# Performance work log

Hardware: AMD Instinct MI355X
Metric: run time of the kernel (lower is better)

The kernel has to match this reference:

```python
import jax, jax.numpy as jnp
import numpy as np

B, N, D_IN, D_OUT = 4, 2048, 1024, 1024


def setup_inputs() -> dict:
    key = jax.random.key(0)
    k0, k1, k2, k3 = jax.random.split(key, 4)
    x = jax.random.normal(k0, (B, N, D_IN), dtype=jnp.float32)
    # torch Linear weight is [out, in]; store transposed [in, out] for x @ W
    W_query = jax.random.normal(k1, (D_IN, D_OUT), dtype=jnp.float32) * (D_IN ** -0.5)
    W_key = jax.random.normal(k2, (D_IN, D_OUT), dtype=jnp.float32) * (D_IN ** -0.5)
    W_value = jax.random.normal(k3, (D_IN, D_OUT), dtype=jnp.float32) * (D_IN ** -0.5)
    return {"x": x, "W_query": W_query, "W_key": W_key, "W_value": W_value}


def reference(x, W_query, W_key, W_value):
    # x: [B, N, D_IN]
    num_tokens = x.shape[1]
    embed_dim = x.shape[2]  # NB: original scales by INPUT embed dim
    q = jnp.einsum('bnd,de->bne', x, W_query)  # [B, N, D_OUT]
    k = jnp.einsum('bnd,de->bne', x, W_key)
    v = jnp.einsum('bnd,de->bne', x, W_value)
    scores = jnp.einsum('bqe,bke->bqk', q, k)  # [B, N, N]
    idx = jnp.arange(num_tokens)
    causal_mask = idx[None, :] > idx[:, None]  # True above diagonal
    scores = jnp.where(causal_mask[None, :, :], -jnp.inf, scores)
    scale = jnp.asarray(embed_dim, scores.dtype) ** 0.5
    attn = jax.nn.softmax(scores / scale, axis=-1)  # dropout p=0 (eval)
    context = jnp.einsum('bqk,bke->bqe', attn, v)  # [B, N, D_OUT]
    return context
```

## Files before the change

### kernel.cpp

```cpp
#include <hip/hip_runtime.h>


typedef __attribute__((ext_vector_type(8))) _Float16 half8;
typedef __attribute__((ext_vector_type(4))) _Float16 half4v;
typedef __attribute__((ext_vector_type(4))) float floatx4;

#define AS1 __attribute__((address_space(1)))
#define AS3 __attribute__((address_space(3)))

__device__ __forceinline__ void load16_lds(void* lds, const void* g) {
  __builtin_amdgcn_global_load_lds((AS1 void*)g, (AS3 void*)lds, 16, 0, 0);
}


__global__ __launch_bounds__(256)
void conv_f32_f16(const float* __restrict__ in, _Float16* __restrict__ out,
                  float* __restrict__ l) {
  if (blockIdx.x < 8192) {
    const int i = (blockIdx.x * 256 + threadIdx.x) << 2;
    float4 v = *(const float4*)(in + i);
    half4v o = { (_Float16)v.x, (_Float16)v.y, (_Float16)v.z, (_Float16)v.w };
    *(half4v*)(out + i) = o;
  } else {
    const int i = ((blockIdx.x - 8192) * 256 + threadIdx.x) << 2;
    *(float4*)(l + i) = float4{0.f, 0.f, 0.f, 0.f};
  }
}

__global__ __launch_bounds__(256)
void transpose_w(const float* __restrict__ W0, const float* __restrict__ W1,
                 const float* __restrict__ W2, _Float16* __restrict__ Wt) {
  const float* W = blockIdx.z == 0 ? W0 : (blockIdx.z == 1 ? W1 : W2);
  _Float16* out = Wt + (long long)blockIdx.z * 1048576;
  __shared__ _Float16 t[32][33];
  const int tx = threadIdx.x, ty = threadIdx.y;
  const int n0 = blockIdx.x << 5, k0 = blockIdx.y << 5;
#pragma unroll
  for (int i = 0; i < 4; ++i)
    t[ty + i * 8][tx] = (_Float16)W[(long long)(k0 + ty + i * 8) * 1024 + n0 + tx];
  __syncthreads();
#pragma unroll
  for (int i = 0; i < 4; ++i)
    out[(long long)(n0 + ty + i * 8) * 1024 + k0 + tx] = t[tx][ty + i * 8];
}

__global__ __launch_bounds__(256)
void gemm_qkv(const _Float16* __restrict__ A, const _Float16* __restrict__ B,
              _Float16* __restrict__ Q, _Float16* __restrict__ Kh,
              _Float16* __restrict__ Vt) {
  const int bm = blockIdx.y, bn = blockIdx.x;
  const _Float16* Ab = A + (long long)bm * 128 * 1024;
  const _Float16* Bb = B + (long long)bn * 128 * 1024;

  __shared__ _Float16 As[128][64];
  __shared__ _Float16 Bs[128][64];

  const int tid = threadIdx.x;
  const int wave = tid >> 6, lane = tid & 63;
  const int quad = lane >> 4, lr = lane & 15;
  const int wm = (wave >> 1) << 6, wn = (wave & 1) << 6;
  const int srow = lane >> 3;
  const int goff = ((lane & 7) ^ srow) << 3;

  floatx4 acc[4][4] = {};
  const _Float16* ga = Ab + (long long)(wave * 8 + srow) * 1024 + goff;
  const _Float16* gb = Bb + (long long)(wave * 8 + srow) * 1024 + goff;

  for (int k0 = 0; k0 < 1024; k0 += 64) {
    __syncthreads();
#pragma unroll
    for (int c = 0; c < 4; ++c) {
      load16_lds(&As[wave * 8 + 32 * c][0], ga + c * 32 * 1024);
      load16_lds(&Bs[wave * 8 + 32 * c][0], gb + c * 32 * 1024);
    }
    ga += 64; gb += 64;
    __syncthreads();

#pragma unroll
    for (int kk = 0; kk < 2; ++kk) {
      half8 af[4], bf[4];
#pragma unroll
      for (int i = 0; i < 4; ++i) {
        const int ra = wm + (i << 4) + lr;
        const int rb = wn + (i << 4) + lr;
        af[i] = *(const half8*)&As[ra][(((kk << 2) + quad) ^ (ra & 7)) << 3];
        bf[i] = *(const half8*)&Bs[rb][(((kk << 2) + quad) ^ (rb & 7)) << 3];
      }
#pragma unroll
      for (int i = 0; i < 4; ++i)
#pragma unroll
        for (int j = 0; j < 4; ++j)
          acc[i][j] = __builtin_amdgcn_mfma_f32_16x16x32_f16(af[i], bf[j], acc[i][j], 0, 0, 0);
    }
  }

  const int colb = bn * 128 + wn + lr;
  const int rowb = bm * 128 + wm + (quad << 2);

  if (bn < 16) {
    _Float16* C = (bn < 8) ? Q : Kh;
    const int cb = colb & 1023;
#pragma unroll
    for (int i = 0; i < 4; ++i)
#pragma unroll
      for (int j = 0; j < 4; ++j)
#pragma unroll
        for (int r = 0; r < 4; ++r)
          C[(long long)(rowb + (i << 4) + r) * 1024 + cb + (j << 4)] =
              (_Float16)acc[i][j][r];
  } else {
    const int b = rowb >> 11;
    const int tb = rowb & 2047;
#pragma unroll
    for (int i = 0; i < 4; ++i) {
      const int tok = tb + (i << 4);
#pragma unroll
      for (int j = 0; j < 4; ++j) {
        const int d = (colb & 1023) + (j << 4);
        half4v v = { (_Float16)acc[i][j][0], (_Float16)acc[i][j][1],
                     (_Float16)acc[i][j][2], (_Float16)acc[i][j][3] };
        *(half4v*)&Vt[(long long)b * 2097152 + (long long)d * 2048 + tok] = v;
      }
    }
  }
}

__global__ __launch_bounds__(256)
void gemm_s_exp(const _Float16* __restrict__ Q, const _Float16* __restrict__ Kh,
                _Float16* __restrict__ P, float* __restrict__ l) {
  int t = blockIdx.x;
  int bm = 0;
  for (;;) { const int c = bm + 1; if (t < c) break; t -= c; ++bm; }
  const int bn = t;
  const int bz = blockIdx.y;

  const _Float16* Ab = Q  + (long long)bz * 2097152 + (long long)bm * 128 * 1024;
  const _Float16* Bb = Kh + (long long)bz * 2097152 + (long long)bn * 128 * 1024;

  __shared__ _Float16 As[128][64];
  __shared__ _Float16 Bs[128][64];

  const int tid = threadIdx.x;
  const int wave = tid >> 6, lane = tid & 63;
  const int quad = lane >> 4, lr = lane & 15;
  const int wm = (wave >> 1) << 6, wn = (wave & 1) << 6;
  const int srow = lane >> 3;
  const int goff = ((lane & 7) ^ srow) << 3;

  floatx4 acc[4][4] = {};
  const _Float16* ga = Ab + (long long)(wave * 8 + srow) * 1024 + goff;
  const _Float16* gb = Bb + (long long)(wave * 8 + srow) * 1024 + goff;

  for (int k0 = 0; k0 < 1024; k0 += 64) {
    __syncthreads();
#pragma unroll
    for (int c = 0; c < 4; ++c) {
      load16_lds(&As[wave * 8 + 32 * c][0], ga + c * 32 * 1024);
      load16_lds(&Bs[wave * 8 + 32 * c][0], gb + c * 32 * 1024);
    }
    ga += 64; gb += 64;
    __syncthreads();

#pragma unroll
    for (int kk = 0; kk < 2; ++kk) {
      half8 af[4], bf[4];
#pragma unroll
      for (int i = 0; i < 4; ++i) {
        const int ra = wm + (i << 4) + lr;
        const int rb = wn + (i << 4) + lr;
        af[i] = *(const half8*)&As[ra][(((kk << 2) + quad) ^ (ra & 7)) << 3];
        bf[i] = *(const half8*)&Bs[rb][(((kk << 2) + quad) ^ (rb & 7)) << 3];
      }
#pragma unroll
      for (int i = 0; i < 4; ++i)
#pragma unroll
        for (int j = 0; j < 4; ++j)
          acc[i][j] = __builtin_amdgcn_mfma_f32_16x16x32_f16(af[i], bf[j], acc[i][j], 0, 0, 0);
    }
  }

  const int colb = bn * 128 + wn + lr;
  const int rowb = bm * 128 + wm + (quad << 2);
  _Float16* Pb = P + (long long)bz * 4194304;
  const float scl = 0.03125f;

  float rs[4][4];
#pragma unroll
  for (int i = 0; i < 4; ++i)
#pragma unroll
    for (int r = 0; r < 4; ++r) rs[i][r] = 0.f;

#pragma unroll
  for (int i = 0; i < 4; ++i)
#pragma unroll
    for (int j = 0; j < 4; ++j)
#pragma unroll
      for (int r = 0; r < 4; ++r) {
        const int q = rowb + (i << 4) + r;
        const int kcol = colb + (j << 4);
        const float pv = (kcol <= q) ? __expf(acc[i][j][r] * scl) : 0.f;
        Pb[(long long)q * 2048 + kcol] = (_Float16)pv;
        rs[i][r] += pv;
      }

#pragma unroll
  for (int i = 0; i < 4; ++i)
#pragma unroll
    for (int r = 0; r < 4; ++r) {
#pragma unroll
      for (int off = 1; off < 16; off <<= 1)
        rs[i][r] += __shfl_xor(rs[i][r], off);
    }
  if (lr == 0) {
    float* lb = l + bz * 2048;
#pragma unroll
    for (int i = 0; i < 4; ++i)
#pragma unroll
      for (int r = 0; r < 4; ++r)
        atomicAdd(&lb[rowb + (i << 4) + r], rs[i][r]);
  }
}

__global__ __launch_bounds__(256)
void gemm_pv(const _Float16* __restrict__ P, const _Float16* __restrict__ Vt,
             const float* __restrict__ l, float* __restrict__ out) {
  const int dn = blockIdx.x;
  const int bm = 15 - blockIdx.y;
  const int bz = blockIdx.z;
  const int Keff = 128 * (bm + 1);

  const _Float16* Ab = P  + (long long)bz * 4194304 + (long long)bm * 128 * 2048;
  const _Float16* Bb = Vt + (long long)bz * 2097152 + (long long)dn * 128 * 2048;

  __shared__ _Float16 As[128][64];
  __shared__ _Float16 Bs[128][64];

  const int tid = threadIdx.x;
  const int wave = tid >> 6, lane = tid & 63;
  const int quad = lane >> 4, lr = lane & 15;
  const int wm = (wave >> 1) << 6, wn = (wave & 1) << 6;
  const int srow = lane >> 3;
  const int goff = ((lane & 7) ^ srow) << 3;

  floatx4 acc[4][4] = {};
  const _Float16* ga = Ab + (long long)(wave * 8 + srow) * 2048 + goff;
  const _Float16* gb = Bb + (long long)(wave * 8 + srow) * 2048 + goff;

  for (int k0 = 0; k0 < Keff; k0 += 64) {
    __syncthreads();
#pragma unroll
    for (int c = 0; c < 4; ++c) {
      load16_lds(&As[wave * 8 + 32 * c][0], ga + (long long)c * 32 * 2048);
      load16_lds(&Bs[wave * 8 + 32 * c][0], gb + (long long)c * 32 * 2048);
    }
    ga += 64; gb += 64;
    __syncthreads();

#pragma unroll
    for (int kk = 0; kk < 2; ++kk) {
      half8 af[4], bf[4];
#pragma unroll
      for (int i = 0; i < 4; ++i) {
        const int ra = wm + (i << 4) + lr;
        const int rb = wn + (i << 4) + lr;
        af[i] = *(const half8*)&As[ra][(((kk << 2) + quad) ^ (ra & 7)) << 3];
        bf[i] = *(const half8*)&Bs[rb][(((kk << 2) + quad) ^ (rb & 7)) << 3];
      }
#pragma unroll
      for (int i = 0; i < 4; ++i)
#pragma unroll
        for (int j = 0; j < 4; ++j)
          acc[i][j] = __builtin_amdgcn_mfma_f32_16x16x32_f16(af[i], bf[j], acc[i][j], 0, 0, 0);
    }
  }

  const int colb = dn * 128 + wn + lr;
  const int rowb = bm * 128 + wm + (quad << 2);
  const float* lb = l + bz * 2048;
  float* Cb = out + (long long)bz * 2097152;

  float linv[4][4];
#pragma unroll
  for (int i = 0; i < 4; ++i)
#pragma unroll
    for (int r = 0; r < 4; ++r)
      linv[i][r] = 1.0f / lb[rowb + (i << 4) + r];

#pragma unroll
  for (int i = 0; i < 4; ++i)
#pragma unroll
    for (int j = 0; j < 4; ++j)
#pragma unroll
      for (int r = 0; r < 4; ++r)
        Cb[(long long)(rowb + (i << 4) + r) * 1024 + colb + (j << 4)] =
            acc[i][j][r] * linv[i][r];
}


extern "C" void kernel_launch(void* const* d_in, const int* in_sizes, int n_in,
                              void* d_out, int out_size, void* d_ws, size_t ws_size,
                              hipStream_t stream) {
  const float* x  = (const float*)d_in[0];
  const float* Wq = (const float*)d_in[1];
  const float* Wk = (const float*)d_in[2];
  const float* Wv = (const float*)d_in[3];
  float* out = (float*)d_out;

  char* ws = (char*)d_ws;
  _Float16* xh = (_Float16*)(ws);
  _Float16* Wt = (_Float16*)(ws + 16777216);
  _Float16* Q  = (_Float16*)(ws + 23068672);
  _Float16* Kh = (_Float16*)(ws + 39845888);
  _Float16* Vt = (_Float16*)(ws + 56623104);
  _Float16* P  = (_Float16*)(ws + 73400320);
  float*    l  = (float*)   (ws + 106954752);

  conv_f32_f16<<<8200, 256, 0, stream>>>(x, xh, l);
  transpose_w<<<dim3(32, 32, 3), dim3(32, 8), 0, stream>>>(Wq, Wk, Wv, Wt);

  gemm_qkv<<<dim3(24, 64), 256, 0, stream>>>(xh, Wt, Q, Kh, Vt);

  gemm_s_exp<<<dim3(136, 4), 256, 0, stream>>>(Q, Kh, P, l);

  gemm_pv<<<dim3(8, 16, 4), 256, 0, stream>>>(P, Vt, l, out);
}
```

Measured before the change: 250.1 us.

## Fuse score-exp and PV GEMMs into one kernel with per-row-block readiness flags

Merges the QK^T/exp kernel and the PV kernel into a single launch. The first 544 blocks compute P tiles and bump a per-(batch, row-block) counter; the remaining blocks spin on that counter before running the PV GEMM. The conv kernel gets one extra block, presumably to zero the counters. This removes a kernel boundary and lets PV work for early row blocks overlap with score computation for later ones. It relies on producer blocks being scheduled before consumers, so spin-waiting could deadlock or waste CUs if dispatch order is not as assumed.

```diff
diff --git a/kernel.cpp b/kernel.cpp
--- a/kernel.cpp
+++ b/kernel.cpp
@@ -126,17 +126,10 @@
 }
 
 __global__ __launch_bounds__(256)
-void gemm_s_exp(const _Float16* __restrict__ Q, const _Float16* __restrict__ Kh,
-                _Float16* __restrict__ P, float* __restrict__ l) {
-  int t = blockIdx.x;
-  int bm = 0;
-  for (;;) { const int c = bm + 1; if (t < c) break; t -= c; ++bm; }
-  const int bn = t;
-  const int bz = blockIdx.y;
-
-  const _Float16* Ab = Q  + (long long)bz * 2097152 + (long long)bm * 128 * 1024;
-  const _Float16* Bb = Kh + (long long)bz * 2097152 + (long long)bn * 128 * 1024;
-
+void attn_sp(const _Float16* __restrict__ Q, const _Float16* __restrict__ Kh,
+             const _Float16* __restrict__ Vt, _Float16* __restrict__ P,
+             float* __restrict__ l, unsigned int* __restrict__ ready,
+             float* __restrict__ out) {
   __shared__ _Float16 As[128][64];
   __shared__ _Float16 Bs[128][64];
 
@@ -148,152 +141,165 @@
   const int goff = ((lane & 7) ^ srow) << 3;
 
   floatx4 acc[4][4] = {};
-  const _Float16* ga = Ab + (long long)(wave * 8 + srow) * 1024 + goff;
-  const _Float16* gb = Bb + (long long)(wave * 8 + srow) * 1024 + goff;
-
-  for (int k0 = 0; k0 < 1024; k0 += 64) {
+
+  if (blockIdx.x < 544) {
+    const int bz = blockIdx.x & 3;
+    int t = blockIdx.x >> 2;
+    int bm = 0;
+    for (;;) { const int c = bm + 1; if (t < c) break; t -= c; ++bm; }
+    const int bn = t;
+
+    const _Float16* Ab = Q  + (long long)bz * 2097152 + (long long)bm * 128 * 1024;
+    const _Float16* Bb = Kh + (long long)bz * 2097152 + (long long)bn * 128 * 1024;
+
+    const _Float16* ga = Ab + (long long)(wave * 8 + srow) * 1024 + goff;
+    const _Float16* gb = Bb + (long long)(wave * 8 + srow) * 1024 + goff;
+
+    for (int k0 = 0; k0 < 1024; k0 += 64) {
+      __syncthreads();
+#pragma unroll
+      for (int c = 0; c < 4; ++c) {
+        load16_lds(&As[wave * 8 + 32 * c][0], ga + c * 32 * 1024);
+        load16_lds(&Bs[wave * 8 + 32 * c][0], gb + c * 32 * 1024);
+      }
+      ga += 64; gb += 64;
+      __syncthreads();
+
+#pragma unroll
+      for (int kk = 0; kk < 2; ++kk) {
+        half8 af[4], bf[4];
+#pragma unroll
+        for (int i = 0; i < 4; ++i) {
+          const int ra = wm + (i << 4) + lr;
+          const int rb = wn + (i << 4) + lr;
+          af[i] = *(const half8*)&As[ra][(((kk << 2) + quad) ^ (ra & 7)) << 3];
+          bf[i] = *(const half8*)&Bs[rb][(((kk << 2) + quad) ^ (rb & 7)) << 3];
+        }
+#pragma unroll
+        for (int i = 0; i < 4; ++i)
+#pragma unroll
+          for (int j = 0; j < 4; ++j)
+            acc[i][j] = __builtin_amdgcn_mfma_f32_16x16x32_f16(af[i], bf[j], acc[i][j], 0, 0, 0);
+      }
+    }
+
+    const int colb = bn * 128 + wn + lr;
+    const int rowb = bm * 128 + wm + (quad << 2);
+    _Float16* Pb = P + (long long)bz * 4194304;
+    const float scl = 0.03125f;
+
+    float rs[4][4];
+#pragma unroll
+    for (int i = 0; i < 4; ++i)
+#pragma unroll
+      for (int r = 0; r < 4; ++r) rs[i][r] = 0.f;
+
+#pragma unroll
+    for (int i = 0; i < 4; ++i)
+#pragma unroll
+      for (int j = 0; j < 4; ++j)
+#pragma unroll
+        for (int r = 0; r < 4; ++r) {
+          const int q = rowb + (i << 4) + r;
+          const int kcol = colb + (j << 4);
+          const float pv = (kcol <= q) ? __expf(acc[i][j][r] * scl) : 0.f;
+          Pb[(long long)q * 2048 + kcol] = (_Float16)pv;
+          rs[i][r] += pv;
+        }
+
+#pragma unroll
+    for (int i = 0; i < 4; ++i)
+#pragma unroll
+      for (int r = 0; r < 4; ++r) {
+#pragma unroll
+        for (int off = 1; off < 16; off <<= 1)
+          rs[i][r] += __shfl_xor(rs[i][r], off);
+      }
+    if (lr == 0) {
+      float* lb = l + bz * 2048;
+#pragma unroll
+      for (int i = 0; i < 4; ++i)
+#pragma unroll
+        for (int r = 0; r < 4; ++r)
+          atomicAdd(&lb[rowb + (i << 4) + r], rs[i][r]);
+    }
+
+    __threadfence();
     __syncthreads();
-#pragma unroll
-    for (int c = 0; c < 4; ++c) {
-      load16_lds(&As[wave * 8 + 32 * c][0], ga + c * 32 * 1024);
-      load16_lds(&Bs[wave * 8 + 32 * c][0], gb + c * 32 * 1024);
-    }
-    ga += 64; gb += 64;
+    if (tid == 0) atomicAdd(&ready[bz * 16 + bm], 1u);
+
+  } else {
+    const int p = blockIdx.x - 544;
+    const int bz = p & 3;
+    const int r0 = p >> 2;
+    const int bm = r0 >> 3;
+    const int dn = r0 & 7;
+    const int Keff = 128 * (bm + 1);
+
+    if (tid == 0) {
+      while (__hip_atomic_load(&ready[bz * 16 + bm], __ATOMIC_ACQUIRE,
+                               __HIP_MEMORY_SCOPE_AGENT) < (unsigned)(bm + 1)) {
+        __builtin_amdgcn_s_sleep(8);
+      }
+    }
     __syncthreads();
-
-#pragma unroll
-    for (int kk = 0; kk < 2; ++kk) {
-      half8 af[4], bf[4];
-#pragma unroll
-      for (int i = 0; i < 4; ++i) {
-        const int ra = wm + (i << 4) + lr;
-        const int rb = wn + (i << 4) + lr;
-        af[i] = *(const half8*)&As[ra][(((kk << 2) + quad) ^ (ra & 7)) << 3];
-        bf[i] = *(const half8*)&Bs[rb][(((kk << 2) + quad) ^ (rb & 7)) << 3];
-      }
-#pragma unroll
-      for (int i = 0; i < 4; ++i)
-#pragma unroll
-        for (int j = 0; j < 4; ++j)
-          acc[i][j] = __builtin_amdgcn_mfma_f32_16x16x32_f16(af[i], bf[j], acc[i][j], 0, 0, 0);
-    }
+    __threadfence();
+
+    const _Float16* Ab = P  + (long long)bz * 4194304 + (long long)bm * 128 * 2048;
+    const _Float16* Bb = Vt + (long long)bz * 2097152 + (long long)dn * 128 * 2048;
+
+    const _Float16* ga = Ab + (long long)(wave * 8 + srow) * 2048 + goff;
+    const _Float16* gb = Bb + (long long)(wave * 8 + srow) * 2048 + goff;
+
+    for (int k0 = 0; k0 < Keff; k0 += 64) {
+      __syncthreads();
+#pragma unroll
+      for (int c = 0; c < 4; ++c) {
+        load16_lds(&As[wave * 8 + 32 * c][0], ga + (long long)c * 32 * 2048);
+        load16_lds(&Bs[wave * 8 + 32 * c][0], gb + (long long)c * 32 * 2048);
+      }
+      ga += 64; gb += 64;
+      __syncthreads();
+
+#pragma unroll
+      for (int kk = 0; kk < 2; ++kk) {
+        half8 af[4], bf[4];
+#pragma unroll
+        for (int i = 0; i < 4; ++i) {
+          const int ra = wm + (i << 4) + lr;
+          const int rb = wn + (i << 4) + lr;
+          af[i] = *(const half8*)&As[ra][(((kk << 2) + quad) ^ (ra & 7)) << 3];
+          bf[i] = *(const half8*)&Bs[rb][(((kk << 2) + quad) ^ (rb & 7)) << 3];
+        }
+#pragma unroll
+        for (int i = 0; i < 4; ++i)
+#pragma unroll
+          for (int j = 0; j < 4; ++j)
+            acc[i][j] = __builtin_amdgcn_mfma_f32_16x16x32_f16(af[i], bf[j], acc[i][j], 0, 0, 0);
+      }
+    }
+
+    const int colb = dn * 128 + wn + lr;
+    const int rowb = bm * 128 + wm + (quad << 2);
+    const float* lb = l + bz * 2048;
+    float* Cb = out + (long long)bz * 2097152;
+
+    float linv[4][4];
+#pragma unroll
+    for (int i = 0; i < 4; ++i)
+#pragma unroll
+      for (int r = 0; r < 4; ++r)
+        linv[i][r] = 1.0f / lb[rowb + (i << 4) + r];
+
+#pragma unroll
+    for (int i = 0; i < 4; ++i)
+#pragma unroll
+      for (int j = 0; j < 4; ++j)
+#pragma unroll
+        for (int r = 0; r < 4; ++r)
+          Cb[(long long)(rowb + (i << 4) + r) * 1024 + colb + (j << 4)] =
+              acc[i][j][r] * linv[i][r];
   }
-
-  const int colb = bn * 128 + wn + lr;
-  const int rowb = bm * 128 + wm + (quad << 2);
-  _Float16* Pb = P + (long long)bz * 4194304;
-  const float scl = 0.03125f;
-
-  float rs[4][4];
-#pragma unroll
-  for (int i = 0; i < 4; ++i)
-#pragma unroll
-    for (int r = 0; r < 4; ++r) rs[i][r] = 0.f;
-
-#pragma unroll
-  for (int i = 0; i < 4; ++i)
-#pragma unroll
-    for (int j = 0; j < 4; ++j)
-#pragma unroll
-      for (int r = 0; r < 4; ++r) {
-        const int q = rowb + (i << 4) + r;
-        const int kcol = colb + (j << 4);
-        const float pv = (kcol <= q) ? __expf(acc[i][j][r] * scl) : 0.f;
-        Pb[(long long)q * 2048 + kcol] = (_Float16)pv;
-        rs[i][r] += pv;
-      }
-
-#pragma unroll
-  for (int i = 0; i < 4; ++i)
-#pragma unroll
-    for (int r = 0; r < 4; ++r) {
-#pragma unroll
-      for (int off = 1; off < 16; off <<= 1)
-        rs[i][r] += __shfl_xor(rs[i][r], off);
-    }
-  if (lr == 0) {
-    float* lb = l + bz * 2048;
-#pragma unroll
-    for (int i = 0; i < 4; ++i)
-#pragma unroll
-      for (int r = 0; r < 4; ++r)
-        atomicAdd(&lb[rowb + (i << 4) + r], rs[i][r]);
-  }
-}
-
-__global__ __launch_bounds__(256)
-void gemm_pv(const _Float16* __restrict__ P, const _Float16* __restrict__ Vt,
-             const float* __restrict__ l, float* __restrict__ out) {
-  const int dn = blockIdx.x;
-  const int bm = 15 - blockIdx.y;
-  const int bz = blockIdx.z;
-  const int Keff = 128 * (bm + 1);
-
-  const _Float16* Ab = P  + (long long)bz * 4194304 + (long long)bm * 128 * 2048;
-  const _Float16* Bb = Vt + (long long)bz * 2097152 + (long long)dn * 128 * 2048;
-
-  __shared__ _Float16 As[128][64];
-  __shared__ _Float16 Bs[128][64];
-
-  const int tid = threadIdx.x;
-  const int wave = tid >> 6, lane = tid & 63;
-  const int quad = lane >> 4, lr = lane & 15;
-  const int wm = (wave >> 1) << 6, wn = (wave & 1) << 6;
-  const int srow = lane >> 3;
-  const int goff = ((lane & 7) ^ srow) << 3;
-
-  floatx4 acc[4][4] = {};
-  const _Float16* ga = Ab + (long long)(wave * 8 + srow) * 2048 + goff;
-  const _Float16* gb = Bb + (long long)(wave * 8 + srow) * 2048 + goff;
-
-  for (int k0 = 0; k0 < Keff; k0 += 64) {
-    __syncthreads();
-#pragma unroll
-    for (int c = 0; c < 4; ++c) {
-      load16_lds(&As[wave * 8 + 32 * c][0], ga + (long long)c * 32 * 2048);
-      load16_lds(&Bs[wave * 8 + 32 * c][0], gb + (long long)c * 32 * 2048);
-    }
-    ga += 64; gb += 64;
-    __syncthreads();
-
-#pragma unroll
-    for (int kk = 0; kk < 2; ++kk) {
-      half8 af[4], bf[4];
-#pragma unroll
-      for (int i = 0; i < 4; ++i) {
-        const int ra = wm + (i << 4) + lr;
-        const int rb = wn + (i << 4) + lr;
-        af[i] = *(const half8*)&As[ra][(((kk << 2) + quad) ^ (ra & 7)) << 3];
-        bf[i] = *(const half8*)&Bs[rb][(((kk << 2) + quad) ^ (rb & 7)) << 3];
-      }
-#pragma unroll
-      for (int i = 0; i < 4; ++i)
-#pragma unroll
-        for (int j = 0; j < 4; ++j)
-          acc[i][j] = __builtin_amdgcn_mfma_f32_16x16x32_f16(af[i], bf[j], acc[i][j], 0, 0, 0);
-    }
-  }
-
-  const int colb = dn * 128 + wn + lr;
-  const int rowb = bm * 128 + wm + (quad << 2);
-  const float* lb = l + bz * 2048;
-  float* Cb = out + (long long)bz * 2097152;
-
-  float linv[4][4];
-#pragma unroll
-  for (int i = 0; i < 4; ++i)
-#pragma unroll
-    for (int r = 0; r < 4; ++r)
-      linv[i][r] = 1.0f / lb[rowb + (i << 4) + r];
-
-#pragma unroll
-  for (int i = 0; i < 4; ++i)
-#pragma unroll
-    for (int j = 0; j < 4; ++j)
-#pragma unroll
-      for (int r = 0; r < 4; ++r)
-        Cb[(long long)(rowb + (i << 4) + r) * 1024 + colb + (j << 4)] =
-            acc[i][j][r] * linv[i][r];
 }
 
 
@@ -314,13 +320,12 @@
   _Float16* Vt = (_Float16*)(ws + 56623104);
   _Float16* P  = (_Float16*)(ws + 73400320);
   float*    l  = (float*)   (ws + 106954752);
-
-  conv_f32_f16<<<8200, 256, 0, stream>>>(x, xh, l);
+  unsigned int* ready = (unsigned int*)(ws + 106954752 + 32768);
+
+  conv_f32_f16<<<8201, 256, 0, stream>>>(x, xh, l);
   transpose_w<<<dim3(32, 32, 3), dim3(32, 8), 0, stream>>>(Wq, Wk, Wv, Wt);
 
   gemm_qkv<<<dim3(24, 64), 256, 0, stream>>>(xh, Wt, Q, Kh, Vt);
 
-  gemm_s_exp<<<dim3(136, 4), 256, 0, stream>>>(Q, Kh, P, l);
-
-  gemm_pv<<<dim3(8, 16, 4), 256, 0, stream>>>(P, Vt, l, out);
-}
+  attn_sp<<<1056, 256, 0, stream>>>(Q, Kh, Vt, P, l, ready, out);
+}
```

New measurement: 342.0 us. 36.7% more time.
